# Performance work log

Hardware: AMD Instinct MI355X
Metric: run time of the kernel (lower is better)

Reference implementation:

```python
import math
import jax, jax.numpy as jnp
import numpy as np

B, T, C = 8, 1024, 512
H = 8
NUM_FRAMES = 128  # num_tokens
NUM_ANIMALS = 8   # num_id; NUM_FRAMES * NUM_ANIMALS == T


def _linear_params(key, fan_in, fan_out):
    kw, kb = jax.random.split(key)
    bound = 1.0 / math.sqrt(fan_in)
    W = jax.random.uniform(kw, (fan_out, fan_in), jnp.float32, -bound, bound)
    b = jax.random.uniform(kb, (fan_out,), jnp.float32, -bound, bound)
    return W, b


def setup_inputs() -> dict:
    key = jax.random.key(0)
    ks = jax.random.split(key, 6)
    x = jax.random.normal(ks[0], (B, T, C), jnp.float32)
    mask = jnp.ones((B, T), jnp.float32)
    Wq, bq = _linear_params(ks[1], C, C)
    Wk, bk = _linear_params(ks[2], C, C)
    Wv, bv = _linear_params(ks[3], C, C)
    Wp, bp = _linear_params(ks[4], C, C)
    return {"x": x, "mask": mask, "Wq": Wq, "bq": bq, "Wk": Wk, "bk": bk,
            "Wv": Wv, "bv": bv, "Wp": Wp, "bp": bp}


def _block_causal_mask():
    # tril over frames, expanded so all animals within a frame attend to all
    # animals of frames <= current frame: kron(tril(F,F), ones(I,I)) -> (T,T)
    tril = jnp.tril(jnp.ones((NUM_FRAMES, NUM_FRAMES), jnp.float32))
    return jnp.kron(tril, jnp.ones((NUM_ANIMALS, NUM_ANIMALS), jnp.float32))


def reference(x, mask, Wq, bq, Wk, bk, Wv, bv, Wp, bp):
    Bx, Tx, Cx = x.shape
    d = Cx // H
    q = (x @ Wq.T + bq).reshape(Bx, Tx, H, d).transpose(0, 2, 1, 3)  # b h t d
    k = (x @ Wk.T + bk).reshape(Bx, Tx, H, d).transpose(0, 2, 1, 3)
    v = (x @ Wv.T + bv).reshape(Bx, Tx, H, d).transpose(0, 2, 1, 3)
    att = jnp.einsum('bhqd,bhkd->bhqk', q, k) * (1.0 / math.sqrt(d))
    m = _block_causal_mask()[None, None] * mask[:, None, None, :]  # (B,1,T,T)
    att = jnp.where(m == 0, -jnp.inf, att)
    att = jax.nn.softmax(att, axis=-1)
    # dropout is identity (pdrop=0.0 / eval mode)
    y = jnp.einsum('bhqk,bhkd->bhqd', att, v)
    y = y.transpose(0, 2, 1, 3).reshape(Bx, Tx, Cx)
    return y @ Wp.T + bp
```

## Files before the change

kernel.cpp:

```cpp
#include <hip/hip_runtime.h>
#include <cstdint>
#include <cstddef>

#define BB 8
#define TT 1024
#define CC 512
#define HH 8
#define DD 64
#define MM (BB*TT)

typedef short s16x4 __attribute__((ext_vector_type(4)));
typedef _Float16 f16x8 __attribute__((ext_vector_type(8)));
typedef float f32x4  __attribute__((ext_vector_type(4)));

__device__ __forceinline__ short f2hs(float f) {
  _Float16 h = (_Float16)f;
  return __builtin_bit_cast(short, h);
}

__device__ __forceinline__ f32x4 mfma16h(f16x8 a, f16x8 b, f32x4 c) {
  return __builtin_amdgcn_mfma_f32_16x16x32_f16(a, b, c, 0, 0, 0);
}

__device__ __forceinline__ void gload_lds16(const void* g, void* l) {
  __builtin_amdgcn_global_load_lds(
      (const __attribute__((address_space(1))) unsigned int*)g,
      (__attribute__((address_space(3))) unsigned int*)l, 16, 0, 0);
}

__global__ void prep_kernel(const float* __restrict__ x,
                            const float* __restrict__ mask,
                            const float* __restrict__ Wq,
                            const float* __restrict__ Wk,
                            const float* __restrict__ Wv,
                            const float* __restrict__ Wp,
                            short* __restrict__ Xh,
                            short* __restrict__ Wqkv,
                            short* __restrict__ Wpc,
                            float* __restrict__ maskAdd) {
  const int NXv = MM * CC / 4;
  const int NWv = CC * CC / 4;
  const int NM = BB * TT;
  int stride = gridDim.x * blockDim.x;
  for (int i = blockIdx.x * blockDim.x + threadIdx.x; i < NXv + 4 * NWv + NM; i += stride) {
    if (i < NXv) {
      int e = i * 4;
      float4 v = *(const float4*)(x + e);
      s16x4 h = {f2hs(v.x), f2hs(v.y), f2hs(v.z), f2hs(v.w)};
      *(s16x4*)(Xh + e) = h;
    } else if (i < NXv + 4 * NWv) {
      int wi = i - NXv;
      int wsel = wi >> 16;
      int idx = wi & 65535;
      int r = idx >> 7, c = (idx & 127) << 2;
      const float* W = (wsel == 0) ? Wq : (wsel == 1) ? Wk : (wsel == 2) ? Wv : Wp;
      float4 v = *(const float4*)(W + (size_t)r * CC + c);
      s16x4 h = {f2hs(v.x), f2hs(v.y), f2hs(v.z), f2hs(v.w)};
      short* dst = (wsel < 3) ? (Wqkv + (size_t)(wsel * 512 + r) * CC + c)
                              : (Wpc + (size_t)r * CC + c);
      *(s16x4*)dst = h;
    } else {
      int mi = i - NXv - 4 * NWv;
      maskAdd[mi] = (mask[mi] == 0.f) ? -1e30f : 0.f;
    }
  }
}

template <int BN, int EPI>
__global__ __launch_bounds__(512, 4) void gemm_kernel(
    const short* __restrict__ A, const short* __restrict__ Bw,
    const float* __restrict__ b0, const float* __restrict__ b1,
    const float* __restrict__ b2,
    short* __restrict__ qo, short* __restrict__ ko, short* __restrict__ vt,
    float* __restrict__ outp) {
  constexpr int MR = 4;
  constexpr int NR = BN / 64;
  constexpr int ABYT = 128 * 128;
  constexpr int TILE = ABYT + BN * 128;
  constexpr int NT = 8;
  constexpr int BL = BN / 64;
  __shared__ __align__(1024) char smem[2 * TILE];

  const int tid = threadIdx.x;
  const int lane = tid & 63;
  const int w = tid >> 6;
  const int wm = w >> 2, wn = w & 3;
  const int l15 = lane & 15, lg = lane >> 4;
  const int lsw = (l15 & 7) << 4;
  const int sr8 = lane >> 3;
  const int scbsw = ((lane & 7) * 16) ^ (sr8 << 4);

  const int rowA = blockIdx.x * 128;
  const int rowB = blockIdx.y * BN;
  const char* Ab = (const char*)A + (size_t)(rowA + sr8) * 1024 + scbsw;
  const char* Bb = (const char*)Bw + (size_t)(rowB + sr8) * 1024 + scbsw;

  f32x4 acc[MR][NR] = {};

  auto STAGE_A = [&](char* dst, int kt) {
#pragma unroll
    for (int g = 0; g < 2; ++g) {
      int r0 = (w * 2 + g) * 8;
      gload_lds16(Ab + (size_t)r0 * 1024 + (size_t)kt * 128, dst + r0 * 128);
    }
  };
  auto STAGE_B = [&](char* dst, int kt) {
#pragma unroll
    for (int g = 0; g < BL; ++g) {
      int r0 = (w * BL + g) * 8;
      gload_lds16(Bb + (size_t)r0 * 1024 + (size_t)kt * 128, dst + ABYT + r0 * 128);
    }
  };
  auto RDA2 = [&](const char* buf, int mh, int kk, f16x8* af) {
#pragma unroll
    for (int i = 0; i < 2; ++i) {
      int row = wm * 64 + (mh * 2 + i) * 16 + l15;
      af[i] = *(const f16x8*)(buf + row * 128 + ((kk * 64 + lg * 16) ^ lsw));
    }
  };
  auto RDBk = [&](const char* buf, int kk, f16x8* bfr) {
#pragma unroll
    for (int j = 0; j < NR; ++j) {
      int row = wn * (BN / 4) + j * 16 + l15;
      bfr[j] = *(const f16x8*)(buf + ABYT + row * 128 + ((kk * 64 + lg * 16) ^ lsw));
    }
  };

  STAGE_A(smem, 0);
  STAGE_B(smem, 0);
  asm volatile("s_waitcnt vmcnt(0)" ::: "memory");
  __builtin_amdgcn_s_barrier();

  for (int t = 0; t < NT; ++t) {
    char* bufp = smem + (t & 1) * TILE;
    char* bufn = smem + ((t + 1) & 1) * TILE;
    f16x8 af[2], bfr[NR];

#define PH(MH)                                                                \
  __builtin_amdgcn_s_barrier();                                               \
  asm volatile("s_waitcnt lgkmcnt(0)" ::: "memory");                          \
  __builtin_amdgcn_sched_barrier(0);                                          \
  __builtin_amdgcn_s_setprio(1);                                              \
  _Pragma("unroll")                                                           \
  for (int i = 0; i < 2; ++i)                                                 \
    _Pragma("unroll")                                                         \
    for (int j = 0; j < NR; ++j)                                              \
      acc[(MH) * 2 + i][j] = mfma16h(af[i], bfr[j], acc[(MH) * 2 + i][j]);    \
  __builtin_amdgcn_s_setprio(0);

    RDBk(bufp, 0, bfr);
    RDA2(bufp, 0, 0, af);
    if (t + 1 < NT) STAGE_A(bufn, t + 1);
    PH(0)
    RDA2(bufp, 1, 0, af);
    if (t + 1 < NT) STAGE_B(bufn, t + 1);
    PH(1)
    RDBk(bufp, 1, bfr);
    RDA2(bufp, 1, 1, af);
    PH(1)
    RDA2(bufp, 0, 1, af);
    PH(0)
#undef PH
    asm volatile("s_waitcnt vmcnt(0)" ::: "memory");
    __builtin_amdgcn_s_barrier();
  }

#pragma unroll
  for (int m = 0; m < MR; ++m) {
    int rbase = rowA + wm * 64 + m * 16 + lg * 4;
#pragma unroll
    for (int n = 0; n < NR; ++n) {
      int col = rowB + wn * (BN / 4) + n * 16 + l15;
#pragma unroll
      for (int j = 0; j < 4; ++j) {
        float v = acc[m][n][j];
        int r = rbase + j;
        if constexpr (EPI == 0) {
          int b = r >> 10, t = r & 1023;
          int wsel = col >> 9, c = col & 511;
          int h = c >> 6, dd = c & 63;
          int bh = b * HH + h;
          if (wsel == 0) {
            qo[((size_t)bh * TT + t) * DD + dd] = f2hs(v + b0[c]);
          } else if (wsel == 1) {
            ko[((size_t)bh * TT + t) * DD + dd] = f2hs(v + b1[c]);
          } else {
            vt[((size_t)bh * DD + dd) * TT + t] = f2hs(v + b2[c]);
          }
        } else {
          outp[(size_t)r * CC + col] = v + b0[col];
        }
      }
    }
  }
}

__global__ __launch_bounds__(512, 2) void attn_kernel(
    const short* __restrict__ q, const short* __restrict__ k,
    const short* __restrict__ vt, const float* __restrict__ maskAdd,
    short* __restrict__ Yh) {
  const int blk = blockIdx.x;
  const int p = blk & 7;
  const int bh = blk >> 3;
  const int b = bh >> 3, h = bh & 7;
  const int qbA = 8 + p;
  const int qbB = 7 - p;
  const int tid = threadIdx.x;
  const int lane = tid & 63;
  const int w = tid >> 6;
  const int wloc = w & 3;
  const int qtile = (w < 4) ? qbA : qbB;
  const int l15 = lane & 15, lg = lane >> 4;
  const int lsw = (l15 & 7) << 4;

  __shared__ short Ks[2][64 * 64];
  __shared__ short Vs[2][64 * 64];
  __shared__ short Pl[8][16 * 64];

  const short* kbh = k + (size_t)bh * TT * DD;
  const short* vbh = vt + (size_t)bh * DD * TT;

  const int srow = tid >> 3;
  const int scb = ((tid & 7) * 16) ^ ((srow & 7) << 4);

  const int qrow = qtile * 64 + wloc * 16 + l15;
  const short* qptr = q + ((size_t)bh * TT + qrow) * DD;
  f16x8 qf0 = *(const f16x8*)(qptr + lg * 8);
  f16x8 qf1 = *(const f16x8*)(qptr + 32 + lg * 8);

  f32x4 yacc[4] = {};
  float mrun = -1e30f, lrun = 0.f;

  gload_lds16((const char*)kbh + (size_t)srow * 128 + scb,
              (char*)&Ks[0][0] + srow * 128);
  gload_lds16((const char*)vbh + (size_t)srow * 2048 + scb,
              (char*)&Vs[0][0] + srow * 128);
  __syncthreads();

  int buf = 0;
  for (int jt = 0; jt <= qbA; ++jt) {
    if (jt < qbA) {
      int nt = jt + 1;
      gload_lds16((const char*)kbh + (size_t)(nt * 64 + srow) * 128 + scb,
                  (char*)&Ks[buf ^ 1][0] + srow * 128);
      gload_lds16((const char*)vbh + (size_t)srow * 2048 + nt * 128 + scb,
                  (char*)&Vs[buf ^ 1][0] + srow * 128);
    }
    if (jt <= qtile) {
      f32x4 mav[4];
#pragma unroll
      for (int n = 0; n < 4; ++n)
        mav[n] = *(const f32x4*)(maskAdd + (size_t)b * TT + jt * 64 + n * 16 + lg * 4);

      f32x4 sacc[4] = {};
      __builtin_amdgcn_s_setprio(1);
#pragma unroll
      for (int c = 0; c < 2; ++c) {
        f16x8 qc = (c == 0) ? qf0 : qf1;
#pragma unroll
        for (int n = 0; n < 4; ++n) {
          int krow = n * 16 + l15;
          const f16x8 kf = *(const f16x8*)((const char*)&Ks[buf][0] + krow * 128 + ((c * 64 + lg * 16) ^ lsw));
          sacc[n] = mfma16h(kf, qc, sacc[n]);
        }
      }
      __builtin_amdgcn_s_setprio(0);
      const int qloc8 = (wloc * 16 + l15) >> 3;
#pragma unroll
      for (int n = 0; n < 4; ++n)
#pragma unroll
        for (int jj = 0; jj < 4; ++jj) {
          float s = sacc[n][jj] * 0.125f + mav[n][jj];
          if (jt == qtile) {
            int kloc = n * 16 + lg * 4 + jj;
            if ((kloc >> 3) > qloc8) s = -1e30f;
          }
          sacc[n][jj] = s;
        }
      float pm = sacc[0][0];
#pragma unroll
      for (int n = 0; n < 4; ++n)
#pragma unroll
        for (int jj = 0; jj < 4; ++jj) pm = fmaxf(pm, sacc[n][jj]);
      pm = fmaxf(pm, __shfl_xor(pm, 16));
      pm = fmaxf(pm, __shfl_xor(pm, 32));
      float mnew = fmaxf(mrun, pm);
      float alpha = __expf(mrun - mnew);
      mrun = mnew;
      float psum = 0.f;
#pragma unroll
      for (int n = 0; n < 4; ++n) {
        float p0 = __expf(sacc[n][0] - mrun);
        float p1 = __expf(sacc[n][1] - mrun);
        float p2 = __expf(sacc[n][2] - mrun);
        float p3 = __expf(sacc[n][3] - mrun);
        psum += (p0 + p1) + (p2 + p3);
        uint2 pw;
        pw.x = (unsigned)(unsigned short)f2hs(p0) | ((unsigned)(unsigned short)f2hs(p1) << 16);
        pw.y = (unsigned)(unsigned short)f2hs(p2) | ((unsigned)(unsigned short)f2hs(p3) << 16);
        *(uint2*)((char*)&Pl[w][0] + l15 * 128 + ((n * 32 + lg * 8) ^ lsw)) = pw;
      }
      psum += __shfl_xor(psum, 16);
      psum += __shfl_xor(psum, 32);
      lrun = lrun * alpha + psum;
      float ab[4];
#pragma unroll
      for (int jj = 0; jj < 4; ++jj) ab[jj] = __shfl(alpha, lg * 4 + jj);
#pragma unroll
      for (int dt = 0; dt < 4; ++dt)
#pragma unroll
        for (int jj = 0; jj < 4; ++jj) yacc[dt][jj] *= ab[jj];
      __builtin_amdgcn_s_setprio(1);
#pragma unroll
      for (int c = 0; c < 2; ++c) {
        const f16x8 pa = *(const f16x8*)((const char*)&Pl[w][0] + l15 * 128 + ((c * 64 + lg * 16) ^ lsw));
#pragma unroll
        for (int dt = 0; dt < 4; ++dt) {
          int vrow = dt * 16 + l15;
          const f16x8 vf = *(const f16x8*)((const char*)&Vs[buf][0] + vrow * 128 + ((c * 64 + lg * 16) ^ lsw));
          yacc[dt] = mfma16h(pa, vf, yacc[dt]);
        }
      }
      __builtin_amdgcn_s_setprio(0);
    }
    __syncthreads();
    buf ^= 1;
  }

  float lb[4];
#pragma unroll
  for (int jj = 0; jj < 4; ++jj) lb[jj] = 1.f / __shfl(lrun, lg * 4 + jj);
#pragma unroll
  for (int dt = 0; dt < 4; ++dt) {
    int col = h * DD + dt * 16 + l15;
#pragma unroll
    for (int jj = 0; jj < 4; ++jj) {
      int row = b * TT + qtile * 64 + wloc * 16 + lg * 4 + jj;
      float y = yacc[dt][jj] * lb[jj];
      Yh[(size_t)row * CC + col] = f2hs(y);
    }
  }
}

extern "C" void kernel_launch(void* const* d_in, const int* in_sizes, int n_in,
                              void* d_out, int out_size, void* d_ws, size_t ws_size,
                              hipStream_t stream) {
  const float* x    = (const float*)d_in[0];
  const float* mask = (const float*)d_in[1];
  const float* Wq   = (const float*)d_in[2];
  const float* bq   = (const float*)d_in[3];
  const float* Wk   = (const float*)d_in[4];
  const float* bk   = (const float*)d_in[5];
  const float* Wv   = (const float*)d_in[6];
  const float* bv   = (const float*)d_in[7];
  const float* Wp   = (const float*)d_in[8];
  const float* bp   = (const float*)d_in[9];
  float* out = (float*)d_out;

  char* ws = (char*)d_ws;
  short* Xh   = (short*)(ws);
  short* Wqkv = (short*)(ws + (size_t)8 * 1048576);
  short* Wpc  = (short*)(ws + (size_t)10 * 1048576);
  short* qo   = (short*)(ws + (size_t)11 * 1048576);
  short* ko   = (short*)(ws + (size_t)19 * 1048576);
  short* vt   = (short*)(ws + (size_t)27 * 1048576);
  short* Yh   = (short*)(ws + (size_t)35 * 1048576);
  float* maskAdd = (float*)(ws + (size_t)43 * 1048576);

  prep_kernel<<<2048, 256, 0, stream>>>(x, mask, Wq, Wk, Wv, Wp, Xh, Wqkv, Wpc, maskAdd);

  gemm_kernel<192, 0><<<dim3(64, 8), 512, 0, stream>>>(
      Xh, Wqkv, bq, bk, bv, qo, ko, vt, nullptr);

  attn_kernel<<<dim3(512), 512, 0, stream>>>(qo, ko, vt, maskAdd, Yh);

  gemm_kernel<128, 1><<<dim3(64, 4), 512, 0, stream>>>(
      Yh, Wpc, bp, nullptr, nullptr, nullptr, nullptr, nullptr, out);
}
```

Before: 81.04 us.

## Fold softmax scale into Q, seed scores with mask, lazily rescale online softmax

```diff
diff --git a/kernel.cpp b/kernel.cpp
--- a/kernel.cpp
+++ b/kernel.cpp
@@ -11,6 +11,7 @@
 
 typedef short s16x4 __attribute__((ext_vector_type(4)));
 typedef _Float16 f16x8 __attribute__((ext_vector_type(8)));
+typedef _Float16 f16x2 __attribute__((ext_vector_type(2)));
 typedef float f32x4  __attribute__((ext_vector_type(4)));
 
 __device__ __forceinline__ short f2hs(float f) {
@@ -181,7 +182,7 @@
           int h = c >> 6, dd = c & 63;
           int bh = b * HH + h;
           if (wsel == 0) {
-            qo[((size_t)bh * TT + t) * DD + dd] = f2hs(v + b0[c]);
+            qo[((size_t)bh * TT + t) * DD + dd] = f2hs((v + b0[c]) * 0.125f);
           } else if (wsel == 1) {
             ko[((size_t)bh * TT + t) * DD + dd] = f2hs(v + b1[c]);
           } else {
@@ -247,12 +248,10 @@
                   (char*)&Vs[buf ^ 1][0] + srow * 128);
     }
     if (jt <= qtile) {
-      f32x4 mav[4];
+      f32x4 sacc[4];
 #pragma unroll
       for (int n = 0; n < 4; ++n)
-        mav[n] = *(const f32x4*)(maskAdd + (size_t)b * TT + jt * 64 + n * 16 + lg * 4);
-
-      f32x4 sacc[4] = {};
+        sacc[n] = *(const f32x4*)(maskAdd + (size_t)b * TT + jt * 64 + n * 16 + lg * 4);
       __builtin_amdgcn_s_setprio(1);
 #pragma unroll
       for (int c = 0; c < 2; ++c) {
@@ -265,28 +264,36 @@
         }
       }
       __builtin_amdgcn_s_setprio(0);
-      const int qloc8 = (wloc * 16 + l15) >> 3;
-#pragma unroll
-      for (int n = 0; n < 4; ++n)
-#pragma unroll
-        for (int jj = 0; jj < 4; ++jj) {
-          float s = sacc[n][jj] * 0.125f + mav[n][jj];
-          if (jt == qtile) {
+      if (jt == qtile) {
+        const int qloc8 = (wloc * 16 + l15) >> 3;
+#pragma unroll
+        for (int n = 0; n < 4; ++n)
+#pragma unroll
+          for (int jj = 0; jj < 4; ++jj) {
             int kloc = n * 16 + lg * 4 + jj;
-            if ((kloc >> 3) > qloc8) s = -1e30f;
+            if ((kloc >> 3) > qloc8) sacc[n][jj] = -1e30f;
           }
-          sacc[n][jj] = s;
-        }
-      float pm = sacc[0][0];
-#pragma unroll
-      for (int n = 0; n < 4; ++n)
-#pragma unroll
-        for (int jj = 0; jj < 4; ++jj) pm = fmaxf(pm, sacc[n][jj]);
-      pm = fmaxf(pm, __shfl_xor(pm, 16));
-      pm = fmaxf(pm, __shfl_xor(pm, 32));
-      float mnew = fmaxf(mrun, pm);
-      float alpha = __expf(mrun - mnew);
-      mrun = mnew;
+      }
+      float t0 = fmaxf(fmaxf(sacc[0][0], sacc[0][1]), fmaxf(sacc[0][2], sacc[0][3]));
+      float t1 = fmaxf(fmaxf(sacc[1][0], sacc[1][1]), fmaxf(sacc[1][2], sacc[1][3]));
+      float t2 = fmaxf(fmaxf(sacc[2][0], sacc[2][1]), fmaxf(sacc[2][2], sacc[2][3]));
+      float t3 = fmaxf(fmaxf(sacc[3][0], sacc[3][1]), fmaxf(sacc[3][2], sacc[3][3]));
+      float pmL = fmaxf(fmaxf(t0, t1), fmaxf(t2, t3));
+      if (!__all(pmL <= mrun + 8.0f)) {
+        float pm = fmaxf(pmL, __shfl_xor(pmL, 16));
+        pm = fmaxf(pm, __shfl_xor(pm, 32));
+        float mnew = fmaxf(mrun, pm);
+        float alpha = __expf(mrun - mnew);
+        mrun = mnew;
+        lrun *= alpha;
+        float ab[4];
+#pragma unroll
+        for (int jj = 0; jj < 4; ++jj) ab[jj] = __shfl(alpha, lg * 4 + jj);
+#pragma unroll
+        for (int dt = 0; dt < 4; ++dt)
+#pragma unroll
+          for (int jj = 0; jj < 4; ++jj) yacc[dt][jj] *= ab[jj];
+      }
       float psum = 0.f;
 #pragma unroll
       for (int n = 0; n < 4; ++n) {
@@ -296,20 +303,13 @@
         float p3 = __expf(sacc[n][3] - mrun);
         psum += (p0 + p1) + (p2 + p3);
         uint2 pw;
-        pw.x = (unsigned)(unsigned short)f2hs(p0) | ((unsigned)(unsigned short)f2hs(p1) << 16);
-        pw.y = (unsigned)(unsigned short)f2hs(p2) | ((unsigned)(unsigned short)f2hs(p3) << 16);
+        pw.x = __builtin_bit_cast(unsigned, __builtin_amdgcn_cvt_pkrtz(p0, p1));
+        pw.y = __builtin_bit_cast(unsigned, __builtin_amdgcn_cvt_pkrtz(p2, p3));
         *(uint2*)((char*)&Pl[w][0] + l15 * 128 + ((n * 32 + lg * 8) ^ lsw)) = pw;
       }
       psum += __shfl_xor(psum, 16);
       psum += __shfl_xor(psum, 32);
-      lrun = lrun * alpha + psum;
-      float ab[4];
-#pragma unroll
-      for (int jj = 0; jj < 4; ++jj) ab[jj] = __shfl(alpha, lg * 4 + jj);
-#pragma unroll
-      for (int dt = 0; dt < 4; ++dt)
-#pragma unroll
-        for (int jj = 0; jj < 4; ++jj) yacc[dt][jj] *= ab[jj];
+      lrun += psum;
       __builtin_amdgcn_s_setprio(1);
 #pragma unroll
       for (int c = 0; c < 2; ++c) {
```

Result: faster. 74.11 us (-8.5%).

## Give each attention wave 32 query rows, fold scale into Q, skip rescales lazily

Applied to the files above, without the earlier changes.

```diff
diff --git a/kernel.cpp b/kernel.cpp
--- a/kernel.cpp
+++ b/kernel.cpp
@@ -181,7 +181,7 @@
           int h = c >> 6, dd = c & 63;
           int bh = b * HH + h;
           if (wsel == 0) {
-            qo[((size_t)bh * TT + t) * DD + dd] = f2hs(v + b0[c]);
+            qo[((size_t)bh * TT + t) * DD + dd] = f2hs((v + b0[c]) * 0.125f);
           } else if (wsel == 1) {
             ko[((size_t)bh * TT + t) * DD + dd] = f2hs(v + b1[c]);
           } else {
@@ -195,7 +195,7 @@
   }
 }
 
-__global__ __launch_bounds__(512, 2) void attn_kernel(
+__global__ __launch_bounds__(256, 3) void attn_kernel(
     const short* __restrict__ q, const short* __restrict__ k,
     const short* __restrict__ vt, const float* __restrict__ maskAdd,
     short* __restrict__ Yh) {
@@ -208,117 +208,147 @@
   const int tid = threadIdx.x;
   const int lane = tid & 63;
   const int w = tid >> 6;
-  const int wloc = w & 3;
-  const int qtile = (w < 4) ? qbA : qbB;
+  const int wloc = w & 1;
+  const int qtile = (w < 2) ? qbA : qbB;
   const int l15 = lane & 15, lg = lane >> 4;
   const int lsw = (l15 & 7) << 4;
 
   __shared__ short Ks[2][64 * 64];
   __shared__ short Vs[2][64 * 64];
-  __shared__ short Pl[8][16 * 64];
+  __shared__ short Pl[4][32 * 64];
 
   const short* kbh = k + (size_t)bh * TT * DD;
   const short* vbh = vt + (size_t)bh * DD * TT;
 
-  const int srow = tid >> 3;
-  const int scb = ((tid & 7) * 16) ^ ((srow & 7) << 4);
-
-  const int qrow = qtile * 64 + wloc * 16 + l15;
-  const short* qptr = q + ((size_t)bh * TT + qrow) * DD;
-  f16x8 qf0 = *(const f16x8*)(qptr + lg * 8);
-  f16x8 qf1 = *(const f16x8*)(qptr + 32 + lg * 8);
-
-  f32x4 yacc[4] = {};
-  float mrun = -1e30f, lrun = 0.f;
-
-  gload_lds16((const char*)kbh + (size_t)srow * 128 + scb,
-              (char*)&Ks[0][0] + srow * 128);
-  gload_lds16((const char*)vbh + (size_t)srow * 2048 + scb,
-              (char*)&Vs[0][0] + srow * 128);
+  const int sr = lane >> 3;
+  const int scbase = (lane & 7) * 16;
+
+  auto STAGE = [&](int bs, int tile) {
+#pragma unroll
+    for (int g = 0; g < 2; ++g) {
+      int row = w * 16 + g * 8 + sr;
+      int swz = (row & 7) << 4;
+      gload_lds16((const char*)kbh + ((size_t)tile * 64 + row) * 128 + (scbase ^ swz),
+                  (char*)&Ks[bs][0] + row * 128);
+      gload_lds16((const char*)vbh + (size_t)row * 2048 + tile * 128 + (scbase ^ swz),
+                  (char*)&Vs[bs][0] + row * 128);
+    }
+  };
+
+  f16x8 qf[2][2];
+#pragma unroll
+  for (int qg = 0; qg < 2; ++qg) {
+    int qrow = qtile * 64 + wloc * 32 + qg * 16 + l15;
+    const short* qptr = q + ((size_t)bh * TT + qrow) * DD;
+    qf[qg][0] = *(const f16x8*)(qptr + lg * 8);
+    qf[qg][1] = *(const f16x8*)(qptr + 32 + lg * 8);
+  }
+
+  f32x4 yacc[2][4] = {};
+  float mrun[2] = {-1e30f, -1e30f}, lrun[2] = {0.f, 0.f};
+
+  STAGE(0, 0);
   __syncthreads();
 
   int buf = 0;
   for (int jt = 0; jt <= qbA; ++jt) {
-    if (jt < qbA) {
-      int nt = jt + 1;
-      gload_lds16((const char*)kbh + (size_t)(nt * 64 + srow) * 128 + scb,
-                  (char*)&Ks[buf ^ 1][0] + srow * 128);
-      gload_lds16((const char*)vbh + (size_t)srow * 2048 + nt * 128 + scb,
-                  (char*)&Vs[buf ^ 1][0] + srow * 128);
-    }
+    if (jt < qbA) STAGE(buf ^ 1, jt + 1);
     if (jt <= qtile) {
       f32x4 mav[4];
 #pragma unroll
       for (int n = 0; n < 4; ++n)
         mav[n] = *(const f32x4*)(maskAdd + (size_t)b * TT + jt * 64 + n * 16 + lg * 4);
-
-      f32x4 sacc[4] = {};
+      f16x8 kf[2][4];
+#pragma unroll
+      for (int c = 0; c < 2; ++c)
+#pragma unroll
+        for (int n = 0; n < 4; ++n)
+          kf[c][n] = *(const f16x8*)((const char*)&Ks[buf][0] + (n * 16 + l15) * 128 +
+                                     ((c * 64 + lg * 16) ^ lsw));
+      f32x4 sacc[2][4];
+#pragma unroll
+      for (int qg = 0; qg < 2; ++qg)
+#pragma unroll
+        for (int n = 0; n < 4; ++n) sacc[qg][n] = mav[n];
       __builtin_amdgcn_s_setprio(1);
 #pragma unroll
+      for (int c = 0; c < 2; ++c)
+#pragma unroll
+        for (int qg = 0; qg < 2; ++qg)
+#pragma unroll
+          for (int n = 0; n < 4; ++n)
+            sacc[qg][n] = mfma16h(kf[c][n], qf[qg][c], sacc[qg][n]);
+      __builtin_amdgcn_s_setprio(0);
+      if (jt == qtile) {
+#pragma unroll
+        for (int qg = 0; qg < 2; ++qg) {
+          const int qloc8 = (wloc * 32 + qg * 16 + l15) >> 3;
+#pragma unroll
+          for (int n = 0; n < 4; ++n)
+#pragma unroll
+            for (int jj = 0; jj < 4; ++jj) {
+              int kloc = n * 16 + lg * 4 + jj;
+              if ((kloc >> 3) > qloc8) sacc[qg][n][jj] = -1e30f;
+            }
+        }
+      }
+      float pmL[2];
+#pragma unroll
+      for (int qg = 0; qg < 2; ++qg) {
+        float t0 = fmaxf(fmaxf(sacc[qg][0][0], sacc[qg][0][1]), fmaxf(sacc[qg][0][2], sacc[qg][0][3]));
+        float t1 = fmaxf(fmaxf(sacc[qg][1][0], sacc[qg][1][1]), fmaxf(sacc[qg][1][2], sacc[qg][1][3]));
+        float t2 = fmaxf(fmaxf(sacc[qg][2][0], sacc[qg][2][1]), fmaxf(sacc[qg][2][2], sacc[qg][2][3]));
+        float t3 = fmaxf(fmaxf(sacc[qg][3][0], sacc[qg][3][1]), fmaxf(sacc[qg][3][2], sacc[qg][3][3]));
+        pmL[qg] = fmaxf(fmaxf(t0, t1), fmaxf(t2, t3));
+      }
+      if (!__all((pmL[0] <= mrun[0] + 8.0f) && (pmL[1] <= mrun[1] + 8.0f))) {
+#pragma unroll
+        for (int qg = 0; qg < 2; ++qg) {
+          float pm = fmaxf(pmL[qg], __shfl_xor(pmL[qg], 16));
+          pm = fmaxf(pm, __shfl_xor(pm, 32));
+          float mnew = fmaxf(mrun[qg], pm);
+          float alpha = __expf(mrun[qg] - mnew);
+          mrun[qg] = mnew;
+          lrun[qg] *= alpha;
+          float ab[4];
+#pragma unroll
+          for (int jj = 0; jj < 4; ++jj) ab[jj] = __shfl(alpha, lg * 4 + jj);
+#pragma unroll
+          for (int dt = 0; dt < 4; ++dt)
+#pragma unroll
+            for (int jj = 0; jj < 4; ++jj) yacc[qg][dt][jj] *= ab[jj];
+        }
+      }
+#pragma unroll
+      for (int qg = 0; qg < 2; ++qg) {
+        float psum = 0.f;
+#pragma unroll
+        for (int n = 0; n < 4; ++n) {
+          float p0 = __expf(sacc[qg][n][0] - mrun[qg]);
+          float p1 = __expf(sacc[qg][n][1] - mrun[qg]);
+          float p2 = __expf(sacc[qg][n][2] - mrun[qg]);
+          float p3 = __expf(sacc[qg][n][3] - mrun[qg]);
+          psum += (p0 + p1) + (p2 + p3);
+          uint2 pw;
+          pw.x = __builtin_bit_cast(unsigned, __builtin_amdgcn_cvt_pkrtz(p0, p1));
+          pw.y = __builtin_bit_cast(unsigned, __builtin_amdgcn_cvt_pkrtz(p2, p3));
+          *(uint2*)((char*)&Pl[w][0] + (qg * 16 + l15) * 128 + ((n * 32 + lg * 8) ^ lsw)) = pw;
+        }
+        psum += __shfl_xor(psum, 16);
+        psum += __shfl_xor(psum, 32);
+        lrun[qg] += psum;
+      }
+      __builtin_amdgcn_s_setprio(1);
+#pragma unroll
       for (int c = 0; c < 2; ++c) {
-        f16x8 qc = (c == 0) ? qf0 : qf1;
-#pragma unroll
-        for (int n = 0; n < 4; ++n) {
-          int krow = n * 16 + l15;
-          const f16x8 kf = *(const f16x8*)((const char*)&Ks[buf][0] + krow * 128 + ((c * 64 + lg * 16) ^ lsw));
-          sacc[n] = mfma16h(kf, qc, sacc[n]);
-        }
-      }
-      __builtin_amdgcn_s_setprio(0);
-      const int qloc8 = (wloc * 16 + l15) >> 3;
-#pragma unroll
-      for (int n = 0; n < 4; ++n)
-#pragma unroll
-        for (int jj = 0; jj < 4; ++jj) {
-          float s = sacc[n][jj] * 0.125f + mav[n][jj];
-          if (jt == qtile) {
-            int kloc = n * 16 + lg * 4 + jj;
-            if ((kloc >> 3) > qloc8) s = -1e30f;
-          }
-          sacc[n][jj] = s;
-        }
-      float pm = sacc[0][0];
-#pragma unroll
-      for (int n = 0; n < 4; ++n)
-#pragma unroll
-        for (int jj = 0; jj < 4; ++jj) pm = fmaxf(pm, sacc[n][jj]);
-      pm = fmaxf(pm, __shfl_xor(pm, 16));
-      pm = fmaxf(pm, __shfl_xor(pm, 32));
-      float mnew = fmaxf(mrun, pm);
-      float alpha = __expf(mrun - mnew);
-      mrun = mnew;
-      float psum = 0.f;
-#pragma unroll
-      for (int n = 0; n < 4; ++n) {
-        float p0 = __expf(sacc[n][0] - mrun);
-        float p1 = __expf(sacc[n][1] - mrun);
-        float p2 = __expf(sacc[n][2] - mrun);
-        float p3 = __expf(sacc[n][3] - mrun);
-        psum += (p0 + p1) + (p2 + p3);
-        uint2 pw;
-        pw.x = (unsigned)(unsigned short)f2hs(p0) | ((unsigned)(unsigned short)f2hs(p1) << 16);
-        pw.y = (unsigned)(unsigned short)f2hs(p2) | ((unsigned)(unsigned short)f2hs(p3) << 16);
-        *(uint2*)((char*)&Pl[w][0] + l15 * 128 + ((n * 32 + lg * 8) ^ lsw)) = pw;
-      }
-      psum += __shfl_xor(psum, 16);
-      psum += __shfl_xor(psum, 32);
-      lrun = lrun * alpha + psum;
-      float ab[4];
-#pragma unroll
-      for (int jj = 0; jj < 4; ++jj) ab[jj] = __shfl(alpha, lg * 4 + jj);
-#pragma unroll
-      for (int dt = 0; dt < 4; ++dt)
-#pragma unroll
-        for (int jj = 0; jj < 4; ++jj) yacc[dt][jj] *= ab[jj];
-      __builtin_amdgcn_s_setprio(1);
-#pragma unroll
-      for (int c = 0; c < 2; ++c) {
-        const f16x8 pa = *(const f16x8*)((const char*)&Pl[w][0] + l15 * 128 + ((c * 64 + lg * 16) ^ lsw));
+        f16x8 pa0 = *(const f16x8*)((const char*)&Pl[w][0] + l15 * 128 + ((c * 64 + lg * 16) ^ lsw));
+        f16x8 pa1 = *(const f16x8*)((const char*)&Pl[w][0] + (16 + l15) * 128 + ((c * 64 + lg * 16) ^ lsw));
 #pragma unroll
         for (int dt = 0; dt < 4; ++dt) {
-          int vrow = dt * 16 + l15;
-          const f16x8 vf = *(const f16x8*)((const char*)&Vs[buf][0] + vrow * 128 + ((c * 64 + lg * 16) ^ lsw));
-          yacc[dt] = mfma16h(pa, vf, yacc[dt]);
+          f16x8 vf = *(const f16x8*)((const char*)&Vs[buf][0] + (dt * 16 + l15) * 128 +
+                                     ((c * 64 + lg * 16) ^ lsw));
+          yacc[0][dt] = mfma16h(pa0, vf, yacc[0][dt]);
+          yacc[1][dt] = mfma16h(pa1, vf, yacc[1][dt]);
         }
       }
       __builtin_amdgcn_s_setprio(0);
@@ -327,17 +357,20 @@
     buf ^= 1;
   }
 
-  float lb[4];
-#pragma unroll
-  for (int jj = 0; jj < 4; ++jj) lb[jj] = 1.f / __shfl(lrun, lg * 4 + jj);
-#pragma unroll
-  for (int dt = 0; dt < 4; ++dt) {
-    int col = h * DD + dt * 16 + l15;
-#pragma unroll
-    for (int jj = 0; jj < 4; ++jj) {
-      int row = b * TT + qtile * 64 + wloc * 16 + lg * 4 + jj;
-      float y = yacc[dt][jj] * lb[jj];
-      Yh[(size_t)row * CC + col] = f2hs(y);
+#pragma unroll
+  for (int qg = 0; qg < 2; ++qg) {
+    float lb[4];
+#pragma unroll
+    for (int jj = 0; jj < 4; ++jj) lb[jj] = 1.f / __shfl(lrun[qg], lg * 4 + jj);
+#pragma unroll
+    for (int dt = 0; dt < 4; ++dt) {
+      int col = h * DD + dt * 16 + l15;
+#pragma unroll
+      for (int jj = 0; jj < 4; ++jj) {
+        int row = b * TT + qtile * 64 + wloc * 32 + qg * 16 + lg * 4 + jj;
+        float y = yacc[qg][dt][jj] * lb[jj];
+        Yh[(size_t)row * CC + col] = f2hs(y);
+      }
     }
   }
 }
@@ -372,7 +405,7 @@
   gemm_kernel<192, 0><<<dim3(64, 8), 512, 0, stream>>>(
       Xh, Wqkv, bq, bk, bv, qo, ko, vt, nullptr);
 
-  attn_kernel<<<dim3(512), 512, 0, stream>>>(qo, ko, vt, maskAdd, Yh);
+  attn_kernel<<<dim3(512), 256, 0, stream>>>(qo, ko, vt, maskAdd, Yh);
 
   gemm_kernel<128, 1><<<dim3(64, 4), 512, 0, stream>>>(
       Yh, Wpc, bp, nullptr, nullptr, nullptr, nullptr, nullptr, out);
```

After: 81.69 us. Within noise of the previous version (+0.8%).
